# Performance work log

Hardware: AMD Instinct MI355X
Metric: run time of the kernel (lower is better)

## Reference

```python
import jax, jax.numpy as jnp
import numpy as np

N_ATOMS = 50000
N_EDGES = 800000
NODE_DIM = 64
EDGE_DIM = 64
FULL_DIM = 2 * NODE_DIM + EDGE_DIM
BN_EPS = 1e-5


def setup_inputs() -> dict:
    key = jax.random.key(0)
    ks = jax.random.split(key, 8)
    atom_features = jax.random.normal(ks[0], (N_ATOMS, NODE_DIM), dtype=jnp.float32)
    edge_features = jax.random.normal(ks[1], (N_EDGES, EDGE_DIM), dtype=jnp.float32)
    edge_indices = jax.random.randint(ks[2], (N_EDGES, 2), 0, N_ATOMS, dtype=jnp.int64)
    lim = 1.0 / np.sqrt(FULL_DIM)
    W_filter = jax.random.uniform(ks[3], (NODE_DIM, FULL_DIM), jnp.float32, -lim, lim)
    b_filter = jax.random.uniform(ks[4], (NODE_DIM,), jnp.float32, -lim, lim)
    W_core = jax.random.uniform(ks[5], (NODE_DIM, FULL_DIM), jnp.float32, -lim, lim)
    b_core = jax.random.uniform(ks[6], (NODE_DIM,), jnp.float32, -lim, lim)
    gamma_filter = jnp.ones((NODE_DIM,), jnp.float32)
    beta_filter = jnp.zeros((NODE_DIM,), jnp.float32)
    gamma_core = jnp.ones((NODE_DIM,), jnp.float32)
    beta_core = jnp.zeros((NODE_DIM,), jnp.float32)
    return {
        "atom_features": atom_features,
        "edge_features": edge_features,
        "W_filter": W_filter, "b_filter": b_filter,
        "gamma_filter": gamma_filter, "beta_filter": beta_filter,
        "W_core": W_core, "b_core": b_core,
        "gamma_core": gamma_core, "beta_core": beta_core,
        "edge_indices": edge_indices,
    }


def _batchnorm(x, gamma, beta):
    # training-mode BN over the edge axis (biased variance, as torch uses for normalization)
    mean = jnp.mean(x, axis=0)
    var = jnp.mean(jnp.square(x - mean), axis=0)
    return (x - mean) * jax.lax.rsqrt(var + BN_EPS) * gamma + beta


def reference(atom_features, edge_features, W_filter, b_filter, gamma_filter,
              beta_filter, W_core, b_core, gamma_core, beta_core, edge_indices):
    src = edge_indices[:, 0]
    dst = edge_indices[:, 1]
    # z_ij: [E, 2*node_dim + edge_dim]
    z = jnp.concatenate([atom_features[dst], atom_features[src], edge_features], axis=1)
    signal = jax.nn.softplus(_batchnorm(z @ W_core.T + b_core, gamma_core, beta_core))
    gate = jax.nn.sigmoid(_batchnorm(z @ W_filter.T + b_filter, gamma_filter, beta_filter))
    message = gate * signal  # [E, node_dim]
    nbr_sumed = jax.ops.segment_sum(message, dst, num_segments=atom_features.shape[0])
    return atom_features + nbr_sumed
```

## Files before the change

### kernel.cpp

```cpp
#include <hip/hip_runtime.h>
#include <hip/hip_bf16.h>
#include <math.h>

#define N_ATOMS   50000
#define N_EDGES   800000
#define KDIM      192
#define BN_EPS    1e-5f

#define TILE_E     64
#define TPB        5
#define NTILES     (N_EDGES / TILE_E)
#define GRID1      (NTILES / TPB)
#define STAT_SLOTS 32
#define ZSTRIDE    200
#define NSCANBLK   ((N_ATOMS + 255) / 256)

typedef __attribute__((ext_vector_type(8))) __bf16 bf16x8;
typedef __attribute__((ext_vector_type(4))) float  f32x4;
typedef __attribute__((ext_vector_type(4))) unsigned short u16x4;

__device__ __forceinline__ ushort f2bf(float f) {
    union { float f; unsigned u; } v; v.f = f;
    unsigned u = v.u;
    return (ushort)((u + 0x7FFFu + ((u >> 16) & 1u)) >> 16);
}
__device__ __forceinline__ float bf2f(unsigned hi16) {
    union { unsigned u; float f; } v; v.u = hi16 << 16; return v.f;
}
__device__ __forceinline__ float msgf(unsigned pv, float sc_c, float sh_c,
                                      float sc_f, float sh_f) {
    float pc = fmaf(bf2f(pv & 0xFFFFu), sc_c, sh_c);
    float pf = fmaf(bf2f(pv >> 16),     sc_f, sh_f);
    float sp = fmaxf(pc, 0.f) + __logf(1.f + __expf(-fabsf(pc)));
    float sg = 1.f / (1.f + __expf(-pf));
    return sp * sg;
}

__device__ __forceinline__ void gather_tile(
    const float* __restrict__ atom, const float* __restrict__ edgef,
    const int* eidxl, int tilebase, ushort* zl, int tid)
{
    const int er = tid >> 4, f4 = tid & 15;
    const float* p[12];
#pragma unroll
    for (int it = 0; it < 12; ++it) {
        const int seg = it >> 2;
        const int e   = (it & 3) * 16 + er;
        const float* srcp;
        if (seg == 0)      srcp = atom  + (size_t)eidxl[2 * e + 1] * 64;
        else if (seg == 1) srcp = atom  + (size_t)eidxl[2 * e] * 64;
        else               srcp = edgef + (size_t)(tilebase + e) * 64;
        p[it] = srcp + f4 * 4;
    }
    f32x4 v[12];
#pragma unroll
    for (int it = 0; it < 12; ++it) {
        if ((it >> 2) == 2) v[it] = __builtin_nontemporal_load((const f32x4*)p[it]);
        else                v[it] = *(const f32x4*)p[it];
    }
#pragma unroll
    for (int it = 0; it < 12; ++it) {
        const int seg = it >> 2;
        const int e   = (it & 3) * 16 + er;
        u16x4 b;
        b.x = f2bf(v[it].x); b.y = f2bf(v[it].y);
        b.z = f2bf(v[it].z); b.w = f2bf(v[it].w);
        *(u16x4*)&zl[e * ZSTRIDE + seg * 64 + f4 * 4] = b;
    }
}

__global__ __launch_bounds__(256) void gemm_stats_store(
    const float* __restrict__ atom, const float* __restrict__ edgef,
    const ushort* __restrict__ Wb, const int* __restrict__ eidx,
    float* __restrict__ stat_partial, unsigned* __restrict__ ws_pre,
    int do_store)
{
    __shared__ __align__(16) ushort zl[TILE_E * ZSTRIDE];
    __shared__ int eidxl[TPB * 128];
    const int tid  = threadIdx.x;
    const int lane = tid & 63, wave = tid >> 6;
    const int ch = wave >> 1, rp = wave & 1;
    const int row = lane & 15, quad = lane >> 4;

    const int base2 = blockIdx.x * TPB * 128;
    for (int i = tid; i < TPB * 128; i += 256) eidxl[i] = eidx[base2 + i];

    bf16x8 bfr[2][2][6];
#pragma unroll
    for (int m = 0; m < 2; ++m)
#pragma unroll
        for (int nt = 0; nt < 2; ++nt)
#pragma unroll
            for (int ks = 0; ks < 6; ++ks)
                bfr[m][nt][ks] = *(const bf16x8*)&Wb[
                    (size_t)(m * 64 + ch * 32 + nt * 16 + row) * KDIM + ks * 32 + quad * 8];

    float s[2][2] = {{0.f, 0.f}, {0.f, 0.f}};
    float q[2][2] = {{0.f, 0.f}, {0.f, 0.f}};

    const int t0 = blockIdx.x * TPB;
    for (int tt = 0; tt < TPB; ++tt) {
        const int tilebase = (t0 + tt) * TILE_E;
        __syncthreads();
        gather_tile(atom, edgef, eidxl + tt * 128, tilebase, zl, tid);
        __syncthreads();
#pragma unroll
        for (int ett = 0; ett < 2; ++ett) {
            const ushort* zb = zl + ((2 * rp + ett) * 16 + row) * ZSTRIDE;
            bf16x8 a[6];
#pragma unroll
            for (int ks = 0; ks < 6; ++ks)
                a[ks] = *(const bf16x8*)&zb[ks * 32 + quad * 8];
            f32x4 acc[2][2];
#pragma unroll
            for (int m = 0; m < 2; ++m)
#pragma unroll
                for (int nt = 0; nt < 2; ++nt)
                    acc[m][nt] = (f32x4){0.f, 0.f, 0.f, 0.f};
#pragma unroll
            for (int ks = 0; ks < 6; ++ks)
#pragma unroll
                for (int m = 0; m < 2; ++m)
#pragma unroll
                    for (int nt = 0; nt < 2; ++nt)
                        acc[m][nt] = __builtin_amdgcn_mfma_f32_16x16x32_bf16(
                            a[ks], bfr[m][nt][ks], acc[m][nt], 0, 0, 0);
#pragma unroll
            for (int nt = 0; nt < 2; ++nt) {
                const int c = ch * 32 + nt * 16 + row;
#pragma unroll
                for (int r = 0; r < 4; ++r) {
                    float vc = acc[0][nt][r], vf = acc[1][nt][r];
                    s[0][nt] += vc; q[0][nt] += vc * vc;
                    s[1][nt] += vf; q[1][nt] += vf * vf;
                    if (do_store) {
                        const int eloc = (2 * rp + ett) * 16 + quad * 4 + r;
                        unsigned pack = (unsigned)f2bf(vc) | ((unsigned)f2bf(vf) << 16);
                        __builtin_nontemporal_store(pack,
                            ws_pre + (size_t)(tilebase + eloc) * 64 + c);
                    }
                }
            }
        }
    }

    float* slot = stat_partial + (size_t)(blockIdx.x & (STAT_SLOTS - 1)) * 256;
#pragma unroll
    for (int m = 0; m < 2; ++m)
#pragma unroll
        for (int nt = 0; nt < 2; ++nt) {
            float sv = s[m][nt], qv = q[m][nt];
            sv += __shfl_xor(sv, 16, 64); sv += __shfl_xor(sv, 32, 64);
            qv += __shfl_xor(qv, 16, 64); qv += __shfl_xor(qv, 32, 64);
            if (lane < 16) {
                int c = ch * 32 + nt * 16 + lane;
                atomicAdd(slot + m * 128 + c, sv);
                atomicAdd(slot + m * 128 + 64 + c, qv);
            }
        }
}

__global__ void finalize_stats(const float* __restrict__ stat_partial,
                               const float* __restrict__ gc, const float* __restrict__ btc,
                               const float* __restrict__ gf, const float* __restrict__ btf,
                               float* __restrict__ params)
{
    int t = threadIdx.x;
    bool isf = t >= 64;
    int j = t & 63;
    float s = 0.f, q = 0.f;
    for (int slot = 0; slot < STAT_SLOTS; slot++) {
        const float* sp = stat_partial + (size_t)slot * 256 + (isf ? 128 : 0);
        s += sp[j];
        q += sp[64 + j];
    }
    float mean = s / (float)N_EDGES;
    float var  = q / (float)N_EDGES - mean * mean;
    float inv  = rsqrtf(var + BN_EPS);
    float gamma = isf ? gf[j] : gc[j];
    float beta  = isf ? btf[j] : btc[j];
    float scale = gamma * inv;
    float shift = beta - mean * scale;
    params[t]       = scale;
    params[128 + t] = shift;
}

__global__ __launch_bounds__(256) void convert_weights(
    const float* __restrict__ Wc, const float* __restrict__ Wf,
    ushort* __restrict__ Wb)
{
    int i = blockIdx.x * 256 + threadIdx.x;
    float v = (i < 64 * KDIM) ? Wc[i] : Wf[i - 64 * KDIM];
    Wb[i] = f2bf(v);
}

__global__ __launch_bounds__(256) void hist_dst(const int* __restrict__ eidx,
                                                unsigned* __restrict__ counts)
{
    int e = blockIdx.x * 256 + threadIdx.x;
    atomicAdd(&counts[eidx[2 * e + 1]], 1u);
}

__global__ __launch_bounds__(256) void scan_a(const unsigned* __restrict__ counts,
                                              unsigned* __restrict__ row_start,
                                              unsigned* __restrict__ blksum)
{
    __shared__ unsigned sh[256];
    const int tid = threadIdx.x;
    const int i = blockIdx.x * 256 + tid;
    unsigned v = (i < N_ATOMS) ? counts[i] : 0u;
    sh[tid] = v;
    __syncthreads();
    for (int off = 1; off < 256; off <<= 1) {
        unsigned t = (tid >= off) ? sh[tid - off] : 0u;
        __syncthreads();
        sh[tid] += t;
        __syncthreads();
    }
    if (i < N_ATOMS) row_start[i] = sh[tid] - v;
    if (tid == 255) blksum[blockIdx.x] = sh[tid];
}

__global__ void scan_b(unsigned* __restrict__ blksum)
{
    __shared__ unsigned sh[256];
    const int tid = threadIdx.x;
    unsigned v = (tid < NSCANBLK) ? blksum[tid] : 0u;
    sh[tid] = v;
    __syncthreads();
    for (int off = 1; off < 256; off <<= 1) {
        unsigned t = (tid >= off) ? sh[tid - off] : 0u;
        __syncthreads();
        sh[tid] += t;
        __syncthreads();
    }
    if (tid < NSCANBLK) blksum[tid] = sh[tid] - v;
}

__global__ __launch_bounds__(256) void init_cursor(unsigned* __restrict__ row_start,
                                                   const unsigned* __restrict__ blksum,
                                                   unsigned* __restrict__ cursors)
{
    int i = blockIdx.x * 256 + threadIdx.x;
    if (i < N_ATOMS) {
        unsigned base = row_start[i] + blksum[i >> 8];
        row_start[i] = base;
        cursors[i]   = base;
    }
    if (i == 0) row_start[N_ATOMS] = N_EDGES;
}

__global__ __launch_bounds__(256) void fill_csr(const int* __restrict__ eidx,
                                                unsigned* __restrict__ cursors,
                                                unsigned* __restrict__ csr)
{
    int e = blockIdx.x * 256 + threadIdx.x;
    int d = eidx[2 * e + 1];
    unsigned pos = atomicAdd(&cursors[d], 1u);
    csr[pos] = (unsigned)e;
}

__global__ __launch_bounds__(256) void bn_act_reduce(
    const unsigned* __restrict__ ws_pre, const unsigned* __restrict__ csr,
    const unsigned* __restrict__ row_start, const float* __restrict__ atom,
    const float* __restrict__ params, float* __restrict__ out)
{
    const int lane = threadIdx.x & 63;
    const int a    = blockIdx.x * 4 + (threadIdx.x >> 6);

    const float sc_c = params[lane],      sh_c = params[128 + lane];
    const float sc_f = params[64 + lane], sh_f = params[192 + lane];

    unsigned j   = row_start[a];
    unsigned end = row_start[a + 1];
    float acc = 0.f;

    for (; j + 4 <= end; j += 4) {
        unsigned e0 = csr[j], e1 = csr[j + 1], e2 = csr[j + 2], e3 = csr[j + 3];
        unsigned p0 = ws_pre[(size_t)e0 * 64 + lane];
        unsigned p1 = ws_pre[(size_t)e1 * 64 + lane];
        unsigned p2 = ws_pre[(size_t)e2 * 64 + lane];
        unsigned p3 = ws_pre[(size_t)e3 * 64 + lane];
        acc += msgf(p0, sc_c, sh_c, sc_f, sh_f);
        acc += msgf(p1, sc_c, sh_c, sc_f, sh_f);
        acc += msgf(p2, sc_c, sh_c, sc_f, sh_f);
        acc += msgf(p3, sc_c, sh_c, sc_f, sh_f);
    }
    for (; j < end; ++j) {
        unsigned e = csr[j];
        acc += msgf(ws_pre[(size_t)e * 64 + lane], sc_c, sh_c, sc_f, sh_f);
    }
    out[(size_t)a * 64 + lane] = atom[(size_t)a * 64 + lane] + acc;
}

__global__ __launch_bounds__(256) void copy_out(const f32x4* __restrict__ src,
                                                f32x4* __restrict__ dst)
{
    int i = blockIdx.x * blockDim.x + threadIdx.x;
    dst[i] = src[i];
}

__global__ __launch_bounds__(256) void apply_scatter_fb(
    const float* __restrict__ atom, const float* __restrict__ edgef,
    const ushort* __restrict__ Wb, const int* __restrict__ eidx,
    const float* __restrict__ params, float* __restrict__ out)
{
    __shared__ __align__(16) ushort zl[TILE_E * ZSTRIDE];
    __shared__ int eidxl[TPB * 128];
    const int tid  = threadIdx.x;
    const int lane = tid & 63, wave = tid >> 6;
    const int ch = wave >> 1, rp = wave & 1;
    const int row = lane & 15, quad = lane >> 4;

    const int base2 = blockIdx.x * TPB * 128;
    for (int i = tid; i < TPB * 128; i += 256) eidxl[i] = eidx[base2 + i];

    bf16x8 bfr[2][2][6];
#pragma unroll
    for (int m = 0; m < 2; ++m)
#pragma unroll
        for (int nt = 0; nt < 2; ++nt)
#pragma unroll
            for (int ks = 0; ks < 6; ++ks)
                bfr[m][nt][ks] = *(const bf16x8*)&Wb[
                    (size_t)(m * 64 + ch * 32 + nt * 16 + row) * KDIM + ks * 32 + quad * 8];

    float scc[2], shc[2], scf[2], shf[2];
#pragma unroll
    for (int nt = 0; nt < 2; ++nt) {
        int c = ch * 32 + nt * 16 + row;
        scc[nt] = params[c];        shc[nt] = params[128 + c];
        scf[nt] = params[64 + c];   shf[nt] = params[192 + c];
    }

    const int t0 = blockIdx.x * TPB;
    for (int tt = 0; tt < TPB; ++tt) {
        const int tilebase = (t0 + tt) * TILE_E;
        __syncthreads();
        gather_tile(atom, edgef, eidxl + tt * 128, tilebase, zl, tid);
        __syncthreads();
#pragma unroll
        for (int ett = 0; ett < 2; ++ett) {
            const ushort* zb = zl + ((2 * rp + ett) * 16 + row) * ZSTRIDE;
            bf16x8 a[6];
#pragma unroll
            for (int ks = 0; ks < 6; ++ks)
                a[ks] = *(const bf16x8*)&zb[ks * 32 + quad * 8];
            f32x4 acc[2][2];
#pragma unroll
            for (int m = 0; m < 2; ++m)
#pragma unroll
                for (int nt = 0; nt < 2; ++nt)
                    acc[m][nt] = (f32x4){0.f, 0.f, 0.f, 0.f};
#pragma unroll
            for (int ks = 0; ks < 6; ++ks)
#pragma unroll
                for (int m = 0; m < 2; ++m)
#pragma unroll
                    for (int nt = 0; nt < 2; ++nt)
                        acc[m][nt] = __builtin_amdgcn_mfma_f32_16x16x32_bf16(
                            a[ks], bfr[m][nt][ks], acc[m][nt], 0, 0, 0);
#pragma unroll
            for (int nt = 0; nt < 2; ++nt) {
                int c = ch * 32 + nt * 16 + row;
#pragma unroll
                for (int r = 0; r < 4; ++r) {
                    float pc = fmaf(acc[0][nt][r], scc[nt], shc[nt]);
                    float pf = fmaf(acc[1][nt][r], scf[nt], shf[nt]);
                    float sp = fmaxf(pc, 0.f) + __logf(1.f + __expf(-fabsf(pc)));
                    float sg = 1.f / (1.f + __expf(-pf));
                    int eloc = (2 * rp + ett) * 16 + quad * 4 + r;
                    int d = eidxl[tt * 128 + 2 * eloc + 1];
                    atomicAdd(out + (size_t)d * 64 + c, sp * sg);
                }
            }
        }
    }
}

extern "C" void kernel_launch(void* const* d_in, const int* in_sizes, int n_in,
                              void* d_out, int out_size, void* d_ws, size_t ws_size,
                              hipStream_t stream)
{
    const float* atom  = (const float*)d_in[0];
    const float* edgef = (const float*)d_in[1];
    const float* Wf    = (const float*)d_in[2];
    const float* gf    = (const float*)d_in[4];
    const float* btf   = (const float*)d_in[5];
    const float* Wc    = (const float*)d_in[6];
    const float* gc    = (const float*)d_in[8];
    const float* btc   = (const float*)d_in[9];
    const int*   eidx  = (const int*)d_in[10];
    float* out = (float*)d_out;

    unsigned* ws_pre       = (unsigned*)d_ws;
    float*    stat_partial = (float*)(ws_pre + (size_t)N_EDGES * 64);
    float*    params       = stat_partial + STAT_SLOTS * 256;
    ushort*   Wb           = (ushort*)(params + 256);
    unsigned* counts       = (unsigned*)(Wb + 2 * 64 * KDIM);
    unsigned* row_start    = counts + N_ATOMS;
    unsigned* blksum       = row_start + N_ATOMS + 1;
    unsigned* cursors      = blksum + 256;
    unsigned* csr          = cursors + N_ATOMS;

    const size_t need_full = (size_t)((char*)(csr + N_EDGES) - (char*)d_ws);
    const int full = (ws_size >= need_full) ? 1 : 0;

    (void)hipMemsetAsync(stat_partial, 0, STAT_SLOTS * 256 * sizeof(float), stream);
    convert_weights<<<(2 * 64 * KDIM) / 256, 256, 0, stream>>>(Wc, Wf, Wb);

    if (full) {
        (void)hipMemsetAsync(counts, 0, N_ATOMS * sizeof(unsigned), stream);
        hist_dst<<<N_EDGES / 256, 256, 0, stream>>>(eidx, counts);
        gemm_stats_store<<<GRID1, 256, 0, stream>>>(atom, edgef, Wb, eidx,
                                                    stat_partial, ws_pre, 1);
        finalize_stats<<<1, 128, 0, stream>>>(stat_partial, gc, btc, gf, btf, params);
        scan_a<<<NSCANBLK, 256, 0, stream>>>(counts, row_start, blksum);
        scan_b<<<1, 256, 0, stream>>>(blksum);
        init_cursor<<<NSCANBLK, 256, 0, stream>>>(row_start, blksum, cursors);
        fill_csr<<<N_EDGES / 256, 256, 0, stream>>>(eidx, cursors, csr);
        bn_act_reduce<<<N_ATOMS / 4, 256, 0, stream>>>(ws_pre, csr, row_start,
                                                       atom, params, out);
    } else {
        gemm_stats_store<<<GRID1, 256, 0, stream>>>(atom, edgef, Wb, eidx,
                                                    stat_partial, ws_pre, 0);
        finalize_stats<<<1, 128, 0, stream>>>(stat_partial, gc, btc, gf, btf, params);
        copy_out<<<(N_ATOMS * 64 / 4) / 256, 256, 0, stream>>>(
            (const f32x4*)atom, (f32x4*)out);
        apply_scatter_fb<<<GRID1, 256, 0, stream>>>(atom, edgef, Wb, eidx,
                                                    params, out);
    }
}
```

Before: 555.1 us.

## Store pre-activations in CSR order and double-buffer the gather tiles

```diff
diff --git a/kernel.cpp b/kernel.cpp
--- a/kernel.cpp
+++ b/kernel.cpp
@@ -36,28 +36,26 @@
     return sp * sg;
 }
 
-__device__ __forceinline__ void gather_tile(
+__device__ __forceinline__ void gather_issue(
     const float* __restrict__ atom, const float* __restrict__ edgef,
-    const int* eidxl, int tilebase, ushort* zl, int tid)
+    const int* __restrict__ eidx, int tilebase, int tid, f32x4* v)
 {
     const int er = tid >> 4, f4 = tid & 15;
-    const float* p[12];
 #pragma unroll
     for (int it = 0; it < 12; ++it) {
         const int seg = it >> 2;
         const int e   = (it & 3) * 16 + er;
         const float* srcp;
-        if (seg == 0)      srcp = atom  + (size_t)eidxl[2 * e + 1] * 64;
-        else if (seg == 1) srcp = atom  + (size_t)eidxl[2 * e] * 64;
+        if (seg == 0)      srcp = atom  + (size_t)eidx[2 * (tilebase + e) + 1] * 64;
+        else if (seg == 1) srcp = atom  + (size_t)eidx[2 * (tilebase + e)] * 64;
         else               srcp = edgef + (size_t)(tilebase + e) * 64;
-        p[it] = srcp + f4 * 4;
-    }
-    f32x4 v[12];
-#pragma unroll
-    for (int it = 0; it < 12; ++it) {
-        if ((it >> 2) == 2) v[it] = __builtin_nontemporal_load((const f32x4*)p[it]);
-        else                v[it] = *(const f32x4*)p[it];
-    }
+        v[it] = *(const f32x4*)(srcp + f4 * 4);
+    }
+}
+
+__device__ __forceinline__ void gather_commit(const f32x4* v, ushort* zl, int tid)
+{
+    const int er = tid >> 4, f4 = tid & 15;
 #pragma unroll
     for (int it = 0; it < 12; ++it) {
         const int seg = it >> 2;
@@ -72,18 +70,20 @@
 __global__ __launch_bounds__(256) void gemm_stats_store(
     const float* __restrict__ atom, const float* __restrict__ edgef,
     const ushort* __restrict__ Wb, const int* __restrict__ eidx,
+    const unsigned* __restrict__ perm,
     float* __restrict__ stat_partial, unsigned* __restrict__ ws_pre,
     int do_store)
 {
-    __shared__ __align__(16) ushort zl[TILE_E * ZSTRIDE];
-    __shared__ int eidxl[TPB * 128];
+    __shared__ __align__(16) ushort zbuf[2][TILE_E * ZSTRIDE];
+    __shared__ unsigned perml[TPB * TILE_E];
     const int tid  = threadIdx.x;
     const int lane = tid & 63, wave = tid >> 6;
     const int ch = wave >> 1, rp = wave & 1;
     const int row = lane & 15, quad = lane >> 4;
 
-    const int base2 = blockIdx.x * TPB * 128;
-    for (int i = tid; i < TPB * 128; i += 256) eidxl[i] = eidx[base2 + i];
+    const int t0 = blockIdx.x * TPB;
+    for (int i = tid; i < TPB * TILE_E; i += 256)
+        perml[i] = perm[t0 * TILE_E + i];
 
     bf16x8 bfr[2][2][6];
 #pragma unroll
@@ -98,12 +98,16 @@
     float s[2][2] = {{0.f, 0.f}, {0.f, 0.f}};
     float q[2][2] = {{0.f, 0.f}, {0.f, 0.f}};
 
-    const int t0 = blockIdx.x * TPB;
+    f32x4 pre[12];
+    gather_issue(atom, edgef, eidx, t0 * TILE_E, tid, pre);
+
     for (int tt = 0; tt < TPB; ++tt) {
-        const int tilebase = (t0 + tt) * TILE_E;
-        __syncthreads();
-        gather_tile(atom, edgef, eidxl + tt * 128, tilebase, zl, tid);
-        __syncthreads();
+        ushort* zl = zbuf[tt & 1];
+        gather_commit(pre, zl, tid);
+        __syncthreads();
+        if (tt + 1 < TPB)
+            gather_issue(atom, edgef, eidx, (t0 + tt + 1) * TILE_E, tid, pre);
+
 #pragma unroll
         for (int ett = 0; ett < 2; ++ett) {
             const ushort* zb = zl + ((2 * rp + ett) * 16 + row) * ZSTRIDE;
@@ -135,9 +139,9 @@
                     s[1][nt] += vf; q[1][nt] += vf * vf;
                     if (do_store) {
                         const int eloc = (2 * rp + ett) * 16 + quad * 4 + r;
+                        const unsigned pos = perml[tt * TILE_E + eloc];
                         unsigned pack = (unsigned)f2bf(vc) | ((unsigned)f2bf(vf) << 16);
-                        __builtin_nontemporal_store(pack,
-                            ws_pre + (size_t)(tilebase + eloc) * 64 + c);
+                        ws_pre[(size_t)pos * 64 + c] = pack;
                     }
                 }
             }
@@ -250,20 +254,19 @@
     if (i == 0) row_start[N_ATOMS] = N_EDGES;
 }
 
-__global__ __launch_bounds__(256) void fill_csr(const int* __restrict__ eidx,
-                                                unsigned* __restrict__ cursors,
-                                                unsigned* __restrict__ csr)
+__global__ __launch_bounds__(256) void fill_perm(const int* __restrict__ eidx,
+                                                 unsigned* __restrict__ cursors,
+                                                 unsigned* __restrict__ perm)
 {
     int e = blockIdx.x * 256 + threadIdx.x;
     int d = eidx[2 * e + 1];
-    unsigned pos = atomicAdd(&cursors[d], 1u);
-    csr[pos] = (unsigned)e;
+    perm[e] = atomicAdd(&cursors[d], 1u);
 }
 
 __global__ __launch_bounds__(256) void bn_act_reduce(
-    const unsigned* __restrict__ ws_pre, const unsigned* __restrict__ csr,
-    const unsigned* __restrict__ row_start, const float* __restrict__ atom,
-    const float* __restrict__ params, float* __restrict__ out)
+    const unsigned* __restrict__ ws_pre, const unsigned* __restrict__ row_start,
+    const float* __restrict__ atom, const float* __restrict__ params,
+    float* __restrict__ out)
 {
     const int lane = threadIdx.x & 63;
     const int a    = blockIdx.x * 4 + (threadIdx.x >> 6);
@@ -271,25 +274,21 @@
     const float sc_c = params[lane],      sh_c = params[128 + lane];
     const float sc_f = params[64 + lane], sh_f = params[192 + lane];
 
-    unsigned j   = row_start[a];
-    unsigned end = row_start[a + 1];
+    const unsigned jb = row_start[a];
+    const unsigned n  = row_start[a + 1] - jb;
+    const unsigned* base = ws_pre + (size_t)jb * 64 + lane;
+
     float acc = 0.f;
-
-    for (; j + 4 <= end; j += 4) {
-        unsigned e0 = csr[j], e1 = csr[j + 1], e2 = csr[j + 2], e3 = csr[j + 3];
-        unsigned p0 = ws_pre[(size_t)e0 * 64 + lane];
-        unsigned p1 = ws_pre[(size_t)e1 * 64 + lane];
-        unsigned p2 = ws_pre[(size_t)e2 * 64 + lane];
-        unsigned p3 = ws_pre[(size_t)e3 * 64 + lane];
-        acc += msgf(p0, sc_c, sh_c, sc_f, sh_f);
-        acc += msgf(p1, sc_c, sh_c, sc_f, sh_f);
-        acc += msgf(p2, sc_c, sh_c, sc_f, sh_f);
-        acc += msgf(p3, sc_c, sh_c, sc_f, sh_f);
-    }
-    for (; j < end; ++j) {
-        unsigned e = csr[j];
-        acc += msgf(ws_pre[(size_t)e * 64 + lane], sc_c, sh_c, sc_f, sh_f);
-    }
+    unsigned k = 0;
+    for (; k + 8 <= n; k += 8) {
+        unsigned p[8];
+#pragma unroll
+        for (int u = 0; u < 8; ++u) p[u] = base[(size_t)(k + u) * 64];
+#pragma unroll
+        for (int u = 0; u < 8; ++u) acc += msgf(p[u], sc_c, sh_c, sc_f, sh_f);
+    }
+    for (; k < n; ++k) acc += msgf(base[(size_t)k * 64], sc_c, sh_c, sc_f, sh_f);
+
     out[(size_t)a * 64 + lane] = atom[(size_t)a * 64 + lane] + acc;
 }
 
@@ -306,15 +305,11 @@
     const float* __restrict__ params, float* __restrict__ out)
 {
     __shared__ __align__(16) ushort zl[TILE_E * ZSTRIDE];
-    __shared__ int eidxl[TPB * 128];
     const int tid  = threadIdx.x;
     const int lane = tid & 63, wave = tid >> 6;
     const int ch = wave >> 1, rp = wave & 1;
     const int row = lane & 15, quad = lane >> 4;
 
-    const int base2 = blockIdx.x * TPB * 128;
-    for (int i = tid; i < TPB * 128; i += 256) eidxl[i] = eidx[base2 + i];
-
     bf16x8 bfr[2][2][6];
 #pragma unroll
     for (int m = 0; m < 2; ++m)
@@ -336,8 +331,10 @@
     const int t0 = blockIdx.x * TPB;
     for (int tt = 0; tt < TPB; ++tt) {
         const int tilebase = (t0 + tt) * TILE_E;
-        __syncthreads();
-        gather_tile(atom, edgef, eidxl + tt * 128, tilebase, zl, tid);
+        f32x4 pre[12];
+        gather_issue(atom, edgef, eidx, tilebase, tid, pre);
+        __syncthreads();
+        gather_commit(pre, zl, tid);
         __syncthreads();
 #pragma unroll
         for (int ett = 0; ett < 2; ++ett) {
@@ -370,7 +367,7 @@
                     float sp = fmaxf(pc, 0.f) + __logf(1.f + __expf(-fabsf(pc)));
                     float sg = 1.f / (1.f + __expf(-pf));
                     int eloc = (2 * rp + ett) * 16 + quad * 4 + r;
-                    int d = eidxl[tt * 128 + 2 * eloc + 1];
+                    int d = eidx[2 * (tilebase + eloc) + 1];
                     atomicAdd(out + (size_t)d * 64 + c, sp * sg);
                 }
             }
@@ -401,9 +398,9 @@
     unsigned* row_start    = counts + N_ATOMS;
     unsigned* blksum       = row_start + N_ATOMS + 1;
     unsigned* cursors      = blksum + 256;
-    unsigned* csr          = cursors + N_ATOMS;
-
-    const size_t need_full = (size_t)((char*)(csr + N_EDGES) - (char*)d_ws);
+    unsigned* perm         = cursors + N_ATOMS;
+
+    const size_t need_full = (size_t)((char*)(perm + N_EDGES) - (char*)d_ws);
     const int full = (ws_size >= need_full) ? 1 : 0;
 
     (void)hipMemsetAsync(stat_partial, 0, STAT_SLOTS * 256 * sizeof(float), stream);
@@ -412,17 +409,18 @@
     if (full) {
         (void)hipMemsetAsync(counts, 0, N_ATOMS * sizeof(unsigned), stream);
         hist_dst<<<N_EDGES / 256, 256, 0, stream>>>(eidx, counts);
-        gemm_stats_store<<<GRID1, 256, 0, stream>>>(atom, edgef, Wb, eidx,
-                                                    stat_partial, ws_pre, 1);
-        finalize_stats<<<1, 128, 0, stream>>>(stat_partial, gc, btc, gf, btf, params);
         scan_a<<<NSCANBLK, 256, 0, stream>>>(counts, row_start, blksum);
         scan_b<<<1, 256, 0, stream>>>(blksum);
         init_cursor<<<NSCANBLK, 256, 0, stream>>>(row_start, blksum, cursors);
-        fill_csr<<<N_EDGES / 256, 256, 0, stream>>>(eidx, cursors, csr);
-        bn_act_reduce<<<N_ATOMS / 4, 256, 0, stream>>>(ws_pre, csr, row_start,
+        fill_perm<<<N_EDGES / 256, 256, 0, stream>>>(eidx, cursors, perm);
+        gemm_stats_store<<<GRID1, 256, 0, stream>>>(atom, edgef, Wb, eidx, perm,
+                                                    stat_partial, ws_pre, 1);
+        finalize_stats<<<1, 128, 0, stream>>>(stat_partial, gc, btc, gf, btf, params);
+        bn_act_reduce<<<N_ATOMS / 4, 256, 0, stream>>>(ws_pre, row_start,
                                                        atom, params, out);
     } else {
         gemm_stats_store<<<GRID1, 256, 0, stream>>>(atom, edgef, Wb, eidx,
+                                                    (unsigned*)counts ,
                                                     stat_partial, ws_pre, 0);
         finalize_stats<<<1, 128, 0, stream>>>(stat_partial, gc, btc, gf, btf, params);
         copy_out<<<(N_ATOMS * 64 / 4) / 256, 256, 0, stream>>>(
```

Measured after the change: 530.9 us. 1.05x faster.
